# Optimization experiments

Hardware: AMD Instinct MI355X
Metric: run time of the kernel (lower is better)

## Reference

```python
import jax, jax.numpy as jnp
import numpy as np

B, C, H, W = 2, 512, 128, 128
L_NUM, HEADS, LEVELS, POINTS = 6, 8, 1, 4
HEAD_DIM = C // HEADS


def setup_inputs() -> dict:
    key = jax.random.key(0)
    ks = jax.random.split(key, 16)
    s = 0.02
    rn = lambda k, shape, scale=s: jax.random.normal(k, shape, jnp.float32) * scale
    return dict(
        bev_feat=jax.random.normal(ks[0], (B, C, H, W), jnp.float32),
        lidar_feat=jax.random.normal(ks[1], (B, C, H, W), jnp.float32),
        Wv=rn(ks[2], (L_NUM, C, C)), bv=jnp.zeros((L_NUM, C), jnp.float32),
        Woff=rn(ks[3], (L_NUM, C, HEADS * LEVELS * POINTS * 2)),
        boff=rn(ks[4], (L_NUM, HEADS * LEVELS * POINTS * 2), 0.5),
        Waw=rn(ks[5], (L_NUM, C, HEADS * LEVELS * POINTS)),
        baw=jnp.zeros((L_NUM, HEADS * LEVELS * POINTS), jnp.float32),
        Wout=rn(ks[6], (L_NUM, C, C)), bout=jnp.zeros((L_NUM, C), jnp.float32),
        ln1_g=jnp.ones((L_NUM, C), jnp.float32), ln1_b=jnp.zeros((L_NUM, C), jnp.float32),
        W1=rn(ks[7], (L_NUM, C, C)), W2=rn(ks[8], (L_NUM, C, C)),
        ln2_g=jnp.ones((L_NUM, C), jnp.float32), ln2_b=jnp.zeros((L_NUM, C), jnp.float32),
        pe_W1=rn(ks[9], (2, C), 0.5),
        pe_bn_g=jnp.ones((C,), jnp.float32), pe_bn_b=jnp.zeros((C,), jnp.float32),
        pe_bn_m=jnp.zeros((C,), jnp.float32), pe_bn_v=jnp.ones((C,), jnp.float32),
        pe_W2=rn(ks[10], (C, C)),
    )


def _layer_norm(x, g, b):
    mu = jnp.mean(x, -1, keepdims=True)
    var = jnp.mean((x - mu) ** 2, -1, keepdims=True)
    return (x - mu) * jax.lax.rsqrt(var + 1e-5) * g + b


def _bilinear_gather(v_flat, locx, locy):
    # v_flat: (B, heads, H*W, d); locx/locy: (B, heads, S) normalized [0,1]
    # grid_sample semantics: align_corners=False, zero padding
    x = locx * W - 0.5
    y = locy * H - 0.5
    x0f = jnp.floor(x); y0f = jnp.floor(y)
    wx = x - x0f; wy = y - y0f
    x0 = x0f.astype(jnp.int32); y0 = y0f.astype(jnp.int32)

    def corner(xi, yi, w):
        inb = (xi >= 0) & (xi < W) & (yi >= 0) & (yi < H)
        idx = jnp.clip(yi, 0, H - 1) * W + jnp.clip(xi, 0, W - 1)
        g = jnp.take_along_axis(v_flat, idx[..., None], axis=2)
        return g * (w * inb)[..., None]

    return (corner(x0, y0, (1 - wx) * (1 - wy)) + corner(x0 + 1, y0, wx * (1 - wy))
            + corner(x0, y0 + 1, (1 - wx) * wy) + corner(x0 + 1, y0 + 1, wx * wy))


def reference(bev_feat, lidar_feat, Wv, bv, Woff, boff, Waw, baw, Wout, bout,
              ln1_g, ln1_b, W1, W2, ln2_g, ln2_b,
              pe_W1, pe_bn_g, pe_bn_b, pe_bn_m, pe_bn_v, pe_W2):
    N = H * W
    # sparse voxelization: keep rows with all-nonzero features, pack valid-first per batch
    lf = jnp.transpose(lidar_feat, (0, 2, 3, 1)).reshape(B, N, C)
    mask = jnp.all(lf != 0, axis=-1)                       # (B,N)
    order = jnp.argsort((~mask).astype(jnp.int32), axis=1, stable=True)  # valid first
    valid = jnp.take_along_axis(mask, order, axis=1)       # (B,N)
    q = jnp.take_along_axis(lf, order[..., None], axis=1) * valid[..., None]
    hh = jnp.arange(N) // W
    ww = jnp.arange(N) % W
    ref_all = jnp.stack([ww / W, hh / H], -1).astype(jnp.float32)  # (N,2) = (x,y)
    ref = jnp.broadcast_to(ref_all, (B, N, 2))
    ref = jnp.take_along_axis(ref, order[..., None], axis=1) * valid[..., None]
    # learned positional embedding (BatchNorm in eval mode)
    pe = ref.reshape(B * N, 2) @ pe_W1
    pe = (pe - pe_bn_m) * jax.lax.rsqrt(pe_bn_v + 1e-5) * pe_bn_g + pe_bn_b
    q_pos = (jax.nn.relu(pe) @ pe_W2).reshape(B, N, C)
    feat_flat = jnp.transpose(bev_feat.reshape(B, C, N), (0, 2, 1))  # (B,N,C)
    norm_xy = jnp.array([W, H], jnp.float32)  # offset normalizer per level (w,h)
    for i in range(L_NUM):
        ident = q
        x = q + q_pos
        v = (feat_flat @ Wv[i] + bv[i]).reshape(B, N, HEADS, HEAD_DIM)
        v_flat = jnp.transpose(v, (0, 2, 1, 3))  # (B,heads,N,d)
        off = (x @ Woff[i] + boff[i]).reshape(B, N, HEADS, LEVELS * POINTS, 2)
        aw = jax.nn.softmax((x @ Waw[i] + baw[i]).reshape(B, N, HEADS, LEVELS * POINTS), axis=-1)
        loc = ref[:, :, None, None, :] + off / norm_xy      # (B,N,heads,P,2)
        locx = jnp.transpose(loc[..., 0], (0, 2, 1, 3)).reshape(B, HEADS, N * POINTS)
        locy = jnp.transpose(loc[..., 1], (0, 2, 1, 3)).reshape(B, HEADS, N * POINTS)
        samp = _bilinear_gather(v_flat, locx, locy).reshape(B, HEADS, N, POINTS, HEAD_DIM)
        awt = jnp.transpose(aw, (0, 2, 1, 3))               # (B,heads,N,P)
        out = jnp.sum(samp * awt[..., None], axis=3)        # (B,heads,N,d)
        out = jnp.transpose(out, (0, 2, 1, 3)).reshape(B, N, C)
        q = out @ Wout[i] + bout[i] + ident                 # dropout in eval = identity
        q = _layer_norm(q, ln1_g[i], ln1_b[i])
        q = jax.nn.relu(q @ W1[i]) @ W2[i] + q
        q = _layer_norm(q, ln2_g[i], ln2_b[i])
    # scatter back to dense (B,C,H,W); invalid voxels stay zero
    slots = jnp.zeros((B, N, C), q.dtype)
    slots = slots.at[jnp.arange(B)[:, None], order].set(q * valid[..., None])
    return jnp.transpose(slots.reshape(B, H, W, C), (0, 3, 1, 2))
```

## Files before the change

kernel.cpp:

```cpp
#include <hip/hip_runtime.h>
#include <cstdint>
#include <cstddef>

#define BDIM 2
#define CDIM 512
#define HDIM 128
#define WDIM 128
#define NDIM (HDIM * WDIM)
#define LNUM 6
#define NHEADS 8
#define HEAD_DIM 64
#define NPTS 4
#define BN_TOT (BDIM * NDIM)

typedef unsigned short u16;
typedef __attribute__((ext_vector_type(8))) short bf16x8;
typedef __attribute__((ext_vector_type(4))) float f32x4;

__device__ __forceinline__ u16 f2bf(float x) {
    unsigned u = __float_as_uint(x);
    u += 0x7fffu + ((u >> 16) & 1u);
    return (u16)(u >> 16);
}
__device__ __forceinline__ float bf2f(u16 h) {
    return __uint_as_float(((unsigned)h) << 16);
}

__device__ __forceinline__ void load_lds16(const void* g, void* l) {
    __builtin_amdgcn_global_load_lds(
        (const __attribute__((address_space(1))) void*)g,
        (__attribute__((address_space(3))) void*)l, 16, 0, 0);
}

__device__ __forceinline__ void wait_vm8() { asm volatile("s_waitcnt vmcnt(8)" ::: "memory"); }
__device__ __forceinline__ void wait_vm5() { asm volatile("s_waitcnt vmcnt(5)" ::: "memory"); }
__device__ __forceinline__ void wait_vm4() { asm volatile("s_waitcnt vmcnt(4)" ::: "memory"); }
__device__ __forceinline__ void wait_vm0() { asm volatile("s_waitcnt vmcnt(0)" ::: "memory"); }
__device__ __forceinline__ void sbar()  { __builtin_amdgcn_s_barrier(); }
__device__ __forceinline__ void spin()  { __builtin_amdgcn_sched_barrier(0); }

__global__ void mask_kernel(const float* __restrict__ lidar, int* __restrict__ mask)
{
    int idx = blockIdx.x * blockDim.x + threadIdx.x;
    if (idx >= BN_TOT) return;
    int b = idx / NDIM;
    int n = idx - b * NDIM;
    const float* p = lidar + (size_t)b * CDIM * NDIM + n;
    int ok = 1;
#pragma unroll 8
    for (int c = 0; c < CDIM; ++c)
        ok &= (p[(size_t)c * NDIM] != 0.0f);
    mask[idx] = ok;
}

__global__ void order_kernel(const int* __restrict__ mask, int* __restrict__ order,
                             int* __restrict__ nvalid)
{
    int b = blockIdx.x;
    const int* m = mask + b * NDIM;
    int* ord = order + b * NDIM;
    __shared__ int part[256];
    __shared__ int totalValid;
    int t = threadIdx.x;
    const int CHUNK = NDIM / 256;
    int base = t * CHUNK;
    int cnt = 0;
    for (int i = 0; i < CHUNK; ++i) cnt += m[base + i];
    part[t] = cnt;
    __syncthreads();
    for (int s = 1; s < 256; s <<= 1) {
        int v = (t >= s) ? part[t - s] : 0;
        __syncthreads();
        part[t] += v;
        __syncthreads();
    }
    if (t == 255) { totalValid = part[255]; nvalid[b] = part[255]; }
    __syncthreads();
    int validBefore = (t == 0) ? 0 : part[t - 1];
    int nv = totalValid;
    for (int i = 0; i < CHUNK; ++i) {
        int n = base + i;
        if (m[n]) { ord[validBefore] = n; validBefore++; }
        else      { int invBefore = n - validBefore; ord[nv + invBefore] = n; }
    }
}

__global__ void ref_kernel(const int* __restrict__ order, const int* __restrict__ nvalid,
                           float* __restrict__ ref)
{
    int idx = blockIdx.x * blockDim.x + threadIdx.x;
    if (idx >= BN_TOT) return;
    int b = idx / NDIM;
    int j = idx - b * NDIM;
    int n = order[idx];
    float flag = (j < nvalid[b]) ? 1.0f : 0.0f;
    int hh = n / WDIM;
    int ww = n - hh * WDIM;
    ref[(size_t)idx * 2 + 0] = ((float)ww / (float)WDIM) * flag;
    ref[(size_t)idx * 2 + 1] = ((float)hh / (float)HDIM) * flag;
}

__global__ void pack_q_kernel(const float* __restrict__ lidar, const int* __restrict__ order,
                              const int* __restrict__ nvalid, u16* __restrict__ q)
{
    __shared__ float tile[32][33];
    __shared__ int ord_s[32];
    int b  = blockIdx.z;
    int j0 = blockIdx.x * 32;
    int c0 = blockIdx.y * 32;
    int tx = threadIdx.x, ty = threadIdx.y;
    if (ty == 0) ord_s[tx] = order[b * NDIM + j0 + tx];
    __syncthreads();
    const float* src = lidar + (size_t)b * CDIM * NDIM;
#pragma unroll
    for (int k = 0; k < 4; ++k) {
        int cl = ty * 4 + k;
        tile[cl][tx] = src[(size_t)(c0 + cl) * NDIM + ord_s[tx]];
    }
    __syncthreads();
    int nv = nvalid[b];
#pragma unroll
    for (int k = 0; k < 4; ++k) {
        int jl = ty * 4 + k;
        int j = j0 + jl;
        float f = (j < nv) ? 1.0f : 0.0f;
        q[((size_t)b * NDIM + j) * CDIM + c0 + tx] = f2bf(tile[tx][jl] * f);
    }
}

__global__ void scatter_kernel(const u16* __restrict__ q, const int* __restrict__ order,
                               const int* __restrict__ nvalid, float* __restrict__ out)
{
    __shared__ float tile[32][33];
    __shared__ int ord_s[32];
    int b  = blockIdx.z;
    int j0 = blockIdx.x * 32;
    int c0 = blockIdx.y * 32;
    int tx = threadIdx.x, ty = threadIdx.y;
    if (ty == 0) ord_s[tx] = order[b * NDIM + j0 + tx];
    __syncthreads();
    int nv = nvalid[b];
#pragma unroll
    for (int k = 0; k < 4; ++k) {
        int jl = ty * 4 + k;
        int j = j0 + jl;
        float f = (j < nv) ? 1.0f : 0.0f;
        tile[jl][tx] = bf2f(q[((size_t)b * NDIM + j) * CDIM + c0 + tx]) * f;
    }
    __syncthreads();
    float* dst = out + (size_t)b * CDIM * NDIM;
#pragma unroll
    for (int k = 0; k < 4; ++k) {
        int cl = ty * 4 + k;
        dst[(size_t)(c0 + cl) * NDIM + ord_s[tx]] = tile[tx][cl];
    }
}

__global__ void tconv_b_kernel(const float* __restrict__ src0, u16* __restrict__ dst0)
{
    __shared__ float t[32][33];
    int z = blockIdx.z;
    const float* src = src0 + (size_t)z * 512 * 512;
    u16* dst = dst0 + (size_t)z * 512 * 512;
    int k0 = blockIdx.x * 32, n0 = blockIdx.y * 32;
    int tx = threadIdx.x, ty = threadIdx.y;
#pragma unroll
    for (int j = 0; j < 4; ++j) {
        int kl = ty * 4 + j;
        t[kl][tx] = src[(size_t)(k0 + kl) * 512 + n0 + tx];
    }
    __syncthreads();
#pragma unroll
    for (int j = 0; j < 4; ++j) {
        int nl = ty * 4 + j;
        dst[(size_t)(n0 + nl) * 512 + k0 + tx] = f2bf(t[tx][nl]);
    }
}

__global__ void tconv_offaw_b_kernel(const float* __restrict__ woff0,
                                     const float* __restrict__ waw0,
                                     u16* __restrict__ dst0)
{
    __shared__ float t[32][33];
    int z = blockIdx.z;
    const float* woff = woff0 + (size_t)z * 512 * 64;
    const float* waw  = waw0 + (size_t)z * 512 * 32;
    u16* dst = dst0 + (size_t)z * 96 * 512;
    int k0 = blockIdx.x * 32, n0 = blockIdx.y * 32;
    int tx = threadIdx.x, ty = threadIdx.y;
#pragma unroll
    for (int j = 0; j < 4; ++j) {
        int kl = ty * 4 + j;
        int n = n0 + tx;
        float v = (n < 64) ? woff[(size_t)(k0 + kl) * 64 + n]
                           : waw[(size_t)(k0 + kl) * 32 + (n - 64)];
        t[kl][tx] = v;
    }
    __syncthreads();
#pragma unroll
    for (int j = 0; j < 4; ++j) {
        int nl = ty * 4 + j;
        dst[(size_t)(n0 + nl) * 512 + k0 + tx] = f2bf(t[tx][nl]);
    }
}

__global__ void bev_conv_kernel(const float* __restrict__ bev, u16* __restrict__ dst)
{
    __shared__ float t[32][33];
    int b  = blockIdx.z;
    int n0 = blockIdx.x * 32;
    int c0 = blockIdx.y * 32;
    int tx = threadIdx.x, ty = threadIdx.y;
    const float* src = bev + (size_t)b * CDIM * NDIM;
#pragma unroll
    for (int j = 0; j < 4; ++j) {
        int cl = ty * 4 + j;
        t[cl][tx] = src[(size_t)(c0 + cl) * NDIM + n0 + tx];
    }
    __syncthreads();
#pragma unroll
    for (int j = 0; j < 4; ++j) {
        int nl = ty * 4 + j;
        dst[((size_t)b * NDIM + n0 + nl) * CDIM + c0 + tx] = f2bf(t[tx][nl]);
    }
}

__global__ void pe_hidden_kernel(const float* __restrict__ ref, const float* __restrict__ W1,
                                 const float* __restrict__ g, const float* __restrict__ bb,
                                 const float* __restrict__ m, const float* __restrict__ v,
                                 u16* __restrict__ out)
{
    int row = blockIdx.x;
    float r0 = ref[(size_t)row * 2 + 0];
    float r1 = ref[(size_t)row * 2 + 1];
    for (int c = threadIdx.x; c < CDIM; c += blockDim.x) {
        float pe = r0 * W1[c] + r1 * W1[CDIM + c];
        pe = (pe - m[c]) * rsqrtf(v[c] + 1e-5f) * g[c] + bb[c];
        out[(size_t)row * CDIM + c] = f2bf(fmaxf(pe, 0.0f));
    }
}

__global__ void add_bf_kernel(const u16* __restrict__ q, const u16* __restrict__ qpos,
                              u16* __restrict__ x)
{
    size_t i = (size_t)blockIdx.x * blockDim.x + threadIdx.x;
    uint4 qa = ((const uint4*)q)[i];
    uint4 pv = ((const uint4*)qpos)[i];
    unsigned qw[4] = {qa.x, qa.y, qa.z, qa.w};
    unsigned pw[4] = {pv.x, pv.y, pv.z, pv.w};
    unsigned rw[4];
#pragma unroll
    for (int k = 0; k < 4; ++k) {
        float a0 = bf2f((u16)(qw[k] & 0xffff)), a1 = bf2f((u16)(qw[k] >> 16));
        float p0 = bf2f((u16)(pw[k] & 0xffff)), p1 = bf2f((u16)(pw[k] >> 16));
        rw[k] = (unsigned)f2bf(a0 + p0) | ((unsigned)f2bf(a1 + p1) << 16);
    }
    uint4 r; r.x = rw[0]; r.y = rw[1]; r.z = rw[2]; r.w = rw[3];
    ((uint4*)x)[i] = r;
}

__global__ __launch_bounds__(256) void gemm_bf16(
    const u16* __restrict__ A, const u16* __restrict__ Bt,
    const float* __restrict__ bias, u16* __restrict__ outB, int relu)
{
    __shared__ u16 As[2][128 * 32];
    __shared__ u16 Bs[2][128 * 32];
    int tid = threadIdx.x;
    int wave = tid >> 6, lane = tid & 63;
    int wr = wave >> 1, wc = wave & 1;
    int quad = lane >> 4, l15 = lane & 15;
    int bm = blockIdx.y * 128, bn = blockIdx.x * 128;

    f32x4 acc[4][4];
#pragma unroll
    for (int i = 0; i < 4; ++i)
#pragma unroll
        for (int j = 0; j < 4; ++j) { f32x4 z = {0.f, 0.f, 0.f, 0.f}; acc[i][j] = z; }

    int ch0 = wave, ch1 = wave + 4;
    const u16* Ag0 = A  + (size_t)(bm + ch0 * 16 + (lane >> 2)) * 512 + (lane & 3) * 8;
    const u16* Ag1 = A  + (size_t)(bm + ch1 * 16 + (lane >> 2)) * 512 + (lane & 3) * 8;
    const u16* Bg0 = Bt + (size_t)(bn + ch0 * 16 + (lane >> 2)) * 512 + (lane & 3) * 8;
    const u16* Bg1 = Bt + (size_t)(bn + ch1 * 16 + (lane >> 2)) * 512 + (lane & 3) * 8;

    load_lds16(Ag0, &As[0][ch0 * 512]);
    load_lds16(Ag1, &As[0][ch1 * 512]);
    load_lds16(Bg0, &Bs[0][ch0 * 512]);
    load_lds16(Bg1, &Bs[0][ch1 * 512]);

    for (int it = 0; it < 16; ++it) {
        sbar();  spin();
        int cur = it & 1, nxt = cur ^ 1;
        if (it < 15) {
            int kn = (it + 1) * 32;
            load_lds16(Ag0 + kn, &As[nxt][ch0 * 512]);
            load_lds16(Ag1 + kn, &As[nxt][ch1 * 512]);
            load_lds16(Bg0 + kn, &Bs[nxt][ch0 * 512]);
            load_lds16(Bg1 + kn, &Bs[nxt][ch1 * 512]);
            wait_vm4();
        } else {
            wait_vm0();
        }
        sbar();  spin();
        bf16x8 av[4], bv[4];
#pragma unroll
        for (int mi = 0; mi < 4; ++mi)
            av[mi] = *(const bf16x8*)&As[cur][(wr * 64 + mi * 16 + l15) * 32 + quad * 8];
#pragma unroll
        for (int ni = 0; ni < 4; ++ni)
            bv[ni] = *(const bf16x8*)&Bs[cur][(wc * 64 + ni * 16 + l15) * 32 + quad * 8];
#pragma unroll
        for (int mi = 0; mi < 4; ++mi)
#pragma unroll
            for (int ni = 0; ni < 4; ++ni)
                acc[mi][ni] = __builtin_amdgcn_mfma_f32_16x16x32_bf16(
                    av[mi], bv[ni], acc[mi][ni], 0, 0, 0);
    }

    int rowb = bm + wr * 64;
    int colb = bn + wc * 64;
#pragma unroll
    for (int mi = 0; mi < 4; ++mi) {
#pragma unroll
        for (int ni = 0; ni < 4; ++ni) {
            int col = colb + ni * 16 + l15;
            float bi = bias ? bias[col] : 0.0f;
#pragma unroll
            for (int r = 0; r < 4; ++r) {
                int row = rowb + mi * 16 + quad * 4 + r;
                float val = acc[mi][ni][r] + bi;
                if (relu) val = fmaxf(val, 0.0f);
                outB[(size_t)row * 512 + col] = f2bf(val);
            }
        }
    }
}

__global__ __launch_bounds__(512) void gemm_ln(
    const u16* __restrict__ A, const u16* __restrict__ Bt,
    const float* __restrict__ bias, const u16* __restrict__ resid,
    const float* __restrict__ g, const float* __restrict__ bta,
    u16* __restrict__ outQ, const u16* __restrict__ qpos, u16* __restrict__ outX)
{
    __shared__ u16 As[2][128 * 32];
    __shared__ u16 Bs[2][512 * 32];
    __shared__ float rs[8][64];
    __shared__ float rq[8][64];
    __shared__ float muL[128], invL[128];

    int tid = threadIdx.x;
    int wv = tid >> 6, lane = tid & 63;
    int quad = lane >> 4, l15 = lane & 15;
    int wr = wv >> 2, wc = wv & 3;
    int bm = blockIdx.x * 128;

    f32x4 acc[4][8];
#pragma unroll
    for (int i = 0; i < 4; ++i)
#pragma unroll
        for (int j = 0; j < 8; ++j) { f32x4 z = {0.f, 0.f, 0.f, 0.f}; acc[i][j] = z; }

    const u16* Ag = A + (size_t)(bm + wv * 16 + (lane >> 2)) * 512 + (lane & 3) * 8;
    const u16* Bg[4];
#pragma unroll
    for (int s = 0; s < 4; ++s)
        Bg[s] = Bt + (size_t)((wv * 4 + s) * 16 + (lane >> 2)) * 512 + (lane & 3) * 8;

    load_lds16(Ag, &As[0][wv * 512]);
#pragma unroll
    for (int s = 0; s < 4; ++s)
        load_lds16(Bg[s], &Bs[0][(wv * 4 + s) * 512]);

    for (int kk = 0; kk < 16; ++kk) {
        sbar();  spin();
        int cur = kk & 1, nxt = cur ^ 1;
        if (kk < 15) {
            int kn = (kk + 1) * 32;
            load_lds16(Ag + kn, &As[nxt][wv * 512]);
#pragma unroll
            for (int s = 0; s < 4; ++s)
                load_lds16(Bg[s] + kn, &Bs[nxt][(wv * 4 + s) * 512]);
            wait_vm5();
        } else {
            wait_vm0();
        }
        sbar();  spin();
        bf16x8 av[4], bv[8];
#pragma unroll
        for (int mi = 0; mi < 4; ++mi)
            av[mi] = *(const bf16x8*)&As[cur][(wr * 64 + mi * 16 + l15) * 32 + quad * 8];
#pragma unroll
        for (int ni = 0; ni < 8; ++ni)
            bv[ni] = *(const bf16x8*)&Bs[cur][(wc * 128 + ni * 16 + l15) * 32 + quad * 8];
#pragma unroll
        for (int mi = 0; mi < 4; ++mi)
#pragma unroll
            for (int ni = 0; ni < 8; ++ni)
                acc[mi][ni] = __builtin_amdgcn_mfma_f32_16x16x32_bf16(
                    av[mi], bv[ni], acc[mi][ni], 0, 0, 0);
    }

    int colb = wc * 128;
    float biasv[8], gv[8], btv[8];
#pragma unroll
    for (int ni = 0; ni < 8; ++ni) {
        int c = colb + ni * 16 + l15;
        biasv[ni] = bias ? bias[c] : 0.0f;
        gv[ni] = g[c];
        btv[ni] = bta[c];
    }
#pragma unroll
    for (int mi = 0; mi < 4; ++mi) {
#pragma unroll
        for (int r = 0; r < 4; ++r) {
            size_t rowoff = (size_t)(bm + wr * 64 + mi * 16 + quad * 4 + r) * 512;
#pragma unroll
            for (int ni = 0; ni < 8; ++ni) {
                int col = colb + ni * 16 + l15;
                acc[mi][ni][r] += biasv[ni] + bf2f(resid[rowoff + col]);
            }
        }
    }
#pragma unroll
    for (int mi = 0; mi < 4; ++mi) {
#pragma unroll
        for (int r = 0; r < 4; ++r) {
            float s = 0.f, s2 = 0.f;
#pragma unroll
            for (int ni = 0; ni < 8; ++ni) {
                s  += acc[mi][ni][r];
                s2 += acc[mi][ni][r] * acc[mi][ni][r];
            }
#pragma unroll
            for (int m = 1; m < 16; m <<= 1) {
                s  += __shfl_xor(s, m, 64);
                s2 += __shfl_xor(s2, m, 64);
            }
            if (l15 == 0) {
                rs[wv][mi * 16 + quad * 4 + r] = s;
                rq[wv][mi * 16 + quad * 4 + r] = s2;
            }
        }
    }
    __syncthreads();
    if (tid < 128) {
        int wrg = tid >> 6, lr = tid & 63;
        float s = 0.f, s2 = 0.f;
#pragma unroll
        for (int w4 = 0; w4 < 4; ++w4) {
            int w = wrg * 4 + w4;
            s += rs[w][lr]; s2 += rq[w][lr];
        }
        float mu = s * (1.0f / 512.0f);
        float var = s2 * (1.0f / 512.0f) - mu * mu;
        muL[tid] = mu;
        invL[tid] = rsqrtf(var + 1e-5f);
    }
    __syncthreads();
#pragma unroll
    for (int mi = 0; mi < 4; ++mi) {
#pragma unroll
        for (int r = 0; r < 4; ++r) {
            int lrow = wr * 64 + mi * 16 + quad * 4 + r;
            float mu = muL[lrow], iv = invL[lrow];
            size_t rowoff = (size_t)(bm + lrow) * 512;
#pragma unroll
            for (int ni = 0; ni < 8; ++ni) {
                int col = colb + ni * 16 + l15;
                float y = (acc[mi][ni][r] - mu) * iv * gv[ni] + btv[ni];
                outQ[rowoff + col] = f2bf(y);
                if (outX)
                    outX[rowoff + col] = f2bf(y + bf2f(qpos[rowoff + col]));
            }
        }
    }
}

__global__ __launch_bounds__(256) void gemm_offaw(
    const u16* __restrict__ A, const u16* __restrict__ Bt,
    const float* __restrict__ boff, const float* __restrict__ baw,
    u16* __restrict__ offb, u16* __restrict__ awb)
{
    __shared__ u16 As[2][128 * 32];
    __shared__ u16 Bs[2][128 * 32];
    int tid = threadIdx.x;
    int wave = tid >> 6, lane = tid & 63;
    int wr = wave >> 1, wc = wave & 1;
    int quad = lane >> 4, l15 = lane & 15;
    int bm = blockIdx.y * 128;

    f32x4 acc[4][4];
#pragma unroll
    for (int i = 0; i < 4; ++i)
#pragma unroll
        for (int j = 0; j < 4; ++j) { f32x4 z = {0.f, 0.f, 0.f, 0.f}; acc[i][j] = z; }

    const u16* Ag[4];
    const u16* Bg[4];
#pragma unroll
    for (int s = 0; s < 4; ++s) {
        Ag[s] = A + (size_t)(bm + wr * 64 + s * 16 + (lane >> 2)) * 512 + (lane & 3) * 8;
        int br = wc * 64 + s * 16 + (lane >> 2);
        if (br > 95) br = 95;
        Bg[s] = Bt + (size_t)br * 512 + (lane & 3) * 8;
    }

#pragma unroll
    for (int s = 0; s < 4; ++s) {
        load_lds16(Ag[s], &As[0][(wr * 4 + s) * 512]);
        load_lds16(Bg[s], &Bs[0][(wc * 4 + s) * 512]);
    }

    for (int it = 0; it < 16; ++it) {
        sbar();
        int cur = it & 1, nxt = cur ^ 1;
        if (it < 15) {
            int kn = (it + 1) * 32;
#pragma unroll
            for (int s = 0; s < 4; ++s) {
                load_lds16(Ag[s] + kn, &As[nxt][(wr * 4 + s) * 512]);
                load_lds16(Bg[s] + kn, &Bs[nxt][(wc * 4 + s) * 512]);
            }
            wait_vm8();
        } else {
            wait_vm0();
        }
        bf16x8 av[4], bv[4];
#pragma unroll
        for (int mi = 0; mi < 4; ++mi)
            av[mi] = *(const bf16x8*)&As[cur][(wr * 64 + mi * 16 + l15) * 32 + quad * 8];
#pragma unroll
        for (int ni = 0; ni < 4; ++ni)
            bv[ni] = *(const bf16x8*)&Bs[cur][(wc * 64 + ni * 16 + l15) * 32 + quad * 8];
#pragma unroll
        for (int mi = 0; mi < 4; ++mi)
#pragma unroll
            for (int ni = 0; ni < 4; ++ni)
                acc[mi][ni] = __builtin_amdgcn_mfma_f32_16x16x32_bf16(
                    av[mi], bv[ni], acc[mi][ni], 0, 0, 0);
    }

    int rowb = bm + wr * 64;
#pragma unroll
    for (int mi = 0; mi < 4; ++mi) {
#pragma unroll
        for (int ni = 0; ni < 4; ++ni) {
            int col = wc * 64 + ni * 16 + l15;
            if (col < 96) {
                float bi = (col < 64) ? boff[col] : baw[col - 64];
#pragma unroll
                for (int r = 0; r < 4; ++r) {
                    int row = rowb + mi * 16 + quad * 4 + r;
                    float val = acc[mi][ni][r] + bi;
                    if (col < 64) offb[(size_t)row * 64 + col] = f2bf(val);
                    else          awb[(size_t)row * 32 + (col - 64)] = f2bf(val);
                }
            }
        }
    }
}

__global__ __launch_bounds__(256) void sample_kernel(
    const float* __restrict__ ref, const u16* __restrict__ off,
    const u16* __restrict__ aw, const u16* __restrict__ v,
    u16* __restrict__ out)
{
    int bj = blockIdx.x * 4 + (threadIdx.x >> 6);
    int lane = threadIdx.x & 63;
    int h  = lane >> 3;
    int d8 = (lane & 7) * 8;
    int b  = bj >> 14;

    float rx = ref[(size_t)bj * 2 + 0];
    float ry = ref[(size_t)bj * 2 + 1];
    uint4 offv = *(const uint4*)(off + (size_t)bj * 64 + h * 8);
    uint2 awv  = *(const uint2*)(aw + (size_t)bj * 32 + h * 4);

    float l0 = bf2f((u16)(awv.x & 0xffff)), l1 = bf2f((u16)(awv.x >> 16));
    float l2 = bf2f((u16)(awv.y & 0xffff)), l3 = bf2f((u16)(awv.y >> 16));
    float mx = fmaxf(fmaxf(l0, l1), fmaxf(l2, l3));
    float e[4];
    e[0] = expf(l0 - mx); e[1] = expf(l1 - mx);
    e[2] = expf(l2 - mx); e[3] = expf(l3 - mx);
    float inv_es = 1.0f / (e[0] + e[1] + e[2] + e[3]);

    const u16* vb = v + (size_t)b * NDIM * CDIM + h * HEAD_DIM + d8;
    float acc[8] = {0.f, 0.f, 0.f, 0.f, 0.f, 0.f, 0.f, 0.f};
    unsigned ow[4] = {offv.x, offv.y, offv.z, offv.w};

#pragma unroll
    for (int p = 0; p < NPTS; ++p) {
        float ox = bf2f((u16)(ow[p] & 0xffff));
        float oy = bf2f((u16)(ow[p] >> 16));
        float X = rx * (float)WDIM + ox - 0.5f;
        float Y = ry * (float)HDIM + oy - 0.5f;
        float x0f = floorf(X), y0f = floorf(Y);
        float wx = X - x0f, wy = Y - y0f;
        int x0 = (int)x0f, y0 = (int)y0f;
        float ep = e[p];
#pragma unroll
        for (int cy = 0; cy < 2; ++cy) {
            int yy = y0 + cy;
            float wyc = cy ? wy : (1.0f - wy);
            int yin = (yy >= 0) & (yy < HDIM);
            int yc = min(max(yy, 0), HDIM - 1);
#pragma unroll
            for (int cx = 0; cx < 2; ++cx) {
                int xx = x0 + cx;
                float wxc = cx ? wx : (1.0f - wx);
                int xin = (xx >= 0) & (xx < WDIM);
                int xc = min(max(xx, 0), WDIM - 1);
                float wgt = ep * wyc * wxc * (float)(yin & xin);
                uint4 vv = *(const uint4*)(vb + (size_t)(yc * WDIM + xc) * CDIM);
                acc[0] += wgt * bf2f((u16)(vv.x & 0xffff));
                acc[1] += wgt * bf2f((u16)(vv.x >> 16));
                acc[2] += wgt * bf2f((u16)(vv.y & 0xffff));
                acc[3] += wgt * bf2f((u16)(vv.y >> 16));
                acc[4] += wgt * bf2f((u16)(vv.z & 0xffff));
                acc[5] += wgt * bf2f((u16)(vv.z >> 16));
                acc[6] += wgt * bf2f((u16)(vv.w & 0xffff));
                acc[7] += wgt * bf2f((u16)(vv.w >> 16));
            }
        }
    }
    uint4 r;
    r.x = (unsigned)f2bf(acc[0] * inv_es) | ((unsigned)f2bf(acc[1] * inv_es) << 16);
    r.y = (unsigned)f2bf(acc[2] * inv_es) | ((unsigned)f2bf(acc[3] * inv_es) << 16);
    r.z = (unsigned)f2bf(acc[4] * inv_es) | ((unsigned)f2bf(acc[5] * inv_es) << 16);
    r.w = (unsigned)f2bf(acc[6] * inv_es) | ((unsigned)f2bf(acc[7] * inv_es) << 16);
    *(uint4*)(out + (size_t)bj * CDIM + h * HEAD_DIM + d8) = r;
}

extern "C" void kernel_launch(void* const* d_in, const int* in_sizes, int n_in,
                              void* d_out, int out_size, void* d_ws, size_t ws_size,
                              hipStream_t stream)
{
    const float* bev   = (const float*)d_in[0];
    const float* lidar = (const float*)d_in[1];
    const float* Wv    = (const float*)d_in[2];
    const float* bv    = (const float*)d_in[3];
    const float* Woff  = (const float*)d_in[4];
    const float* boff  = (const float*)d_in[5];
    const float* Waw   = (const float*)d_in[6];
    const float* baw   = (const float*)d_in[7];
    const float* Wout  = (const float*)d_in[8];
    const float* bout  = (const float*)d_in[9];
    const float* ln1g  = (const float*)d_in[10];
    const float* ln1b  = (const float*)d_in[11];
    const float* W1    = (const float*)d_in[12];
    const float* W2    = (const float*)d_in[13];
    const float* ln2g  = (const float*)d_in[14];
    const float* ln2b  = (const float*)d_in[15];
    const float* peW1  = (const float*)d_in[16];
    const float* peg   = (const float*)d_in[17];
    const float* peb   = (const float*)d_in[18];
    const float* pem   = (const float*)d_in[19];
    const float* pev   = (const float*)d_in[20];
    const float* peW2  = (const float*)d_in[21];

    const size_t NC = (size_t)BN_TOT * CDIM;
    const size_t WSZ = 512 * 512;

    char* base = (char*)d_ws;
    u16* q      = (u16*)base;
    u16* actA   = (u16*)(base + NC * 2);
    u16* actB   = (u16*)(base + NC * 4);
    u16* wt     = (u16*)(base + NC * 6);
    u16* wtv    = wt;
    u16* wtout  = wt + 6 * WSZ;
    u16* wt1    = wt + 12 * WSZ;
    u16* wt2    = wt + 18 * WSZ;
    u16* wtpe   = wt + 24 * WSZ;
    u16* offawt = wt + 25 * WSZ;
    u16* offb   = offawt + 6 * 96 * 512;
    u16* awb    = offb + (size_t)BN_TOT * 64;
    float* refb = (float*)(awb + (size_t)BN_TOT * 32);
    int* mask   = (int*)(refb + (size_t)BN_TOT * 2);
    int* order  = mask + BN_TOT;
    int* nvalid = order + BN_TOT;

    u16* qpos_bf = (u16*)d_out;
    u16* featT   = (u16*)d_out + NC;

    dim3 blk328(32, 8);
    dim3 gemm_grid(4, 256);
    dim3 offaw_grid(1, 256);
    int  ln_grid = BN_TOT / 128;

    mask_kernel<<<BN_TOT / 256, 256, 0, stream>>>(lidar, mask);
    order_kernel<<<BDIM, 256, 0, stream>>>(mask, order, nvalid);
    ref_kernel<<<BN_TOT / 256, 256, 0, stream>>>(order, nvalid, refb);
    pack_q_kernel<<<dim3(NDIM / 32, CDIM / 32, BDIM), blk328, 0, stream>>>(lidar, order, nvalid, q);
    bev_conv_kernel<<<dim3(NDIM / 32, CDIM / 32, BDIM), blk328, 0, stream>>>(bev, featT);

    tconv_b_kernel<<<dim3(16, 16, 6), blk328, 0, stream>>>(Wv,   wtv);
    tconv_b_kernel<<<dim3(16, 16, 6), blk328, 0, stream>>>(Wout, wtout);
    tconv_b_kernel<<<dim3(16, 16, 6), blk328, 0, stream>>>(W1,   wt1);
    tconv_b_kernel<<<dim3(16, 16, 6), blk328, 0, stream>>>(W2,   wt2);
    tconv_b_kernel<<<dim3(16, 16, 1), blk328, 0, stream>>>(peW2, wtpe);
    tconv_offaw_b_kernel<<<dim3(16, 3, 6), blk328, 0, stream>>>(Woff, Waw, offawt);

    pe_hidden_kernel<<<BN_TOT, 128, 0, stream>>>(refb, peW1, peg, peb, pem, pev, actA);
    gemm_bf16<<<gemm_grid, 256, 0, stream>>>(actA, wtpe, nullptr, qpos_bf, 0);

    add_bf_kernel<<<(unsigned)(NC / 8 / 256), 256, 0, stream>>>(q, qpos_bf, actB);

    for (int i = 0; i < LNUM; ++i) {
        gemm_offaw<<<offaw_grid, 256, 0, stream>>>(actB, offawt + (size_t)i * 96 * 512,
                                                   boff + i * 64, baw + i * 32, offb, awb);
        gemm_bf16<<<gemm_grid, 256, 0, stream>>>(featT, wtv + (size_t)i * WSZ,
                                                 bv + i * CDIM, actA, 0);
        sample_kernel<<<BN_TOT / 4, 256, 0, stream>>>(refb, offb, awb, actA, actB);
        gemm_ln<<<ln_grid, 512, 0, stream>>>(actB, wtout + (size_t)i * WSZ, bout + i * CDIM,
                                             q, ln1g + i * CDIM, ln1b + i * CDIM,
                                             q, nullptr, nullptr);
        gemm_bf16<<<gemm_grid, 256, 0, stream>>>(q, wt1 + (size_t)i * WSZ, nullptr, actA, 1);
        gemm_ln<<<ln_grid, 512, 0, stream>>>(actA, wt2 + (size_t)i * WSZ, nullptr,
                                             q, ln2g + i * CDIM, ln2b + i * CDIM,
                                             q, qpos_bf,
                                             (i < LNUM - 1) ? actB : nullptr);
    }

    scatter_kernel<<<dim3(NDIM / 32, CDIM / 32, BDIM), blk328, 0, stream>>>(
        q, order, nvalid, (float*)d_out);
}
```

Measured before the change: 1.875 ms.

## Split fused GEMM+LayerNorm into tiled GEMM with fp32 output plus row LayerNorm kernel

Replaces the full-row 128x512 GEMM+LayerNorm kernel, which used 512 threads and a large register tile, with a standard 128x128-tiled GEMM that adds bias and residual and writes fp32. A separate wave-per-row LayerNorm kernel then normalizes the rows and writes bf16 q. The work is split into two halves so the fp32 scratch fits in the existing bf16 activation buffers. The qpos add becomes a separate add kernel. This trades the old kernel's low occupancy and only 256 blocks for higher GEMM parallelism, at the cost of extra fp32 global round-trips and more launches.

```diff
diff --git a/kernel.cpp b/kernel.cpp
--- a/kernel.cpp
+++ b/kernel.cpp
@@ -33,7 +33,6 @@
 }
 
 __device__ __forceinline__ void wait_vm8() { asm volatile("s_waitcnt vmcnt(8)" ::: "memory"); }
-__device__ __forceinline__ void wait_vm5() { asm volatile("s_waitcnt vmcnt(5)" ::: "memory"); }
 __device__ __forceinline__ void wait_vm4() { asm volatile("s_waitcnt vmcnt(4)" ::: "memory"); }
 __device__ __forceinline__ void wait_vm0() { asm volatile("s_waitcnt vmcnt(0)" ::: "memory"); }
 __device__ __forceinline__ void sbar()  { __builtin_amdgcn_s_barrier(); }
@@ -336,144 +335,124 @@
     }
 }
 
-__global__ __launch_bounds__(512) void gemm_ln(
+__global__ __launch_bounds__(256) void gemm_residf(
     const u16* __restrict__ A, const u16* __restrict__ Bt,
     const float* __restrict__ bias, const u16* __restrict__ resid,
-    const float* __restrict__ g, const float* __restrict__ bta,
-    u16* __restrict__ outQ, const u16* __restrict__ qpos, u16* __restrict__ outX)
+    float* __restrict__ outY)
 {
     __shared__ u16 As[2][128 * 32];
-    __shared__ u16 Bs[2][512 * 32];
-    __shared__ float rs[8][64];
-    __shared__ float rq[8][64];
-    __shared__ float muL[128], invL[128];
-
+    __shared__ u16 Bs[2][128 * 32];
     int tid = threadIdx.x;
-    int wv = tid >> 6, lane = tid & 63;
+    int wave = tid >> 6, lane = tid & 63;
+    int wr = wave >> 1, wc = wave & 1;
     int quad = lane >> 4, l15 = lane & 15;
-    int wr = wv >> 2, wc = wv & 3;
-    int bm = blockIdx.x * 128;
-
-    f32x4 acc[4][8];
+    int bm = blockIdx.y * 128, bn = blockIdx.x * 128;
+
+    f32x4 acc[4][4];
 #pragma unroll
     for (int i = 0; i < 4; ++i)
 #pragma unroll
-        for (int j = 0; j < 8; ++j) { f32x4 z = {0.f, 0.f, 0.f, 0.f}; acc[i][j] = z; }
-
-    const u16* Ag = A + (size_t)(bm + wv * 16 + (lane >> 2)) * 512 + (lane & 3) * 8;
-    const u16* Bg[4];
-#pragma unroll
-    for (int s = 0; s < 4; ++s)
-        Bg[s] = Bt + (size_t)((wv * 4 + s) * 16 + (lane >> 2)) * 512 + (lane & 3) * 8;
-
-    load_lds16(Ag, &As[0][wv * 512]);
-#pragma unroll
-    for (int s = 0; s < 4; ++s)
-        load_lds16(Bg[s], &Bs[0][(wv * 4 + s) * 512]);
-
-    for (int kk = 0; kk < 16; ++kk) {
+        for (int j = 0; j < 4; ++j) { f32x4 z = {0.f, 0.f, 0.f, 0.f}; acc[i][j] = z; }
+
+    int ch0 = wave, ch1 = wave + 4;
+    const u16* Ag0 = A  + (size_t)(bm + ch0 * 16 + (lane >> 2)) * 512 + (lane & 3) * 8;
+    const u16* Ag1 = A  + (size_t)(bm + ch1 * 16 + (lane >> 2)) * 512 + (lane & 3) * 8;
+    const u16* Bg0 = Bt + (size_t)(bn + ch0 * 16 + (lane >> 2)) * 512 + (lane & 3) * 8;
+    const u16* Bg1 = Bt + (size_t)(bn + ch1 * 16 + (lane >> 2)) * 512 + (lane & 3) * 8;
+
+    load_lds16(Ag0, &As[0][ch0 * 512]);
+    load_lds16(Ag1, &As[0][ch1 * 512]);
+    load_lds16(Bg0, &Bs[0][ch0 * 512]);
+    load_lds16(Bg1, &Bs[0][ch1 * 512]);
+
+    for (int it = 0; it < 16; ++it) {
         sbar();  spin();
-        int cur = kk & 1, nxt = cur ^ 1;
-        if (kk < 15) {
-            int kn = (kk + 1) * 32;
-            load_lds16(Ag + kn, &As[nxt][wv * 512]);
-#pragma unroll
-            for (int s = 0; s < 4; ++s)
-                load_lds16(Bg[s] + kn, &Bs[nxt][(wv * 4 + s) * 512]);
-            wait_vm5();
+        int cur = it & 1, nxt = cur ^ 1;
+        if (it < 15) {
+            int kn = (it + 1) * 32;
+            load_lds16(Ag0 + kn, &As[nxt][ch0 * 512]);
+            load_lds16(Ag1 + kn, &As[nxt][ch1 * 512]);
+            load_lds16(Bg0 + kn, &Bs[nxt][ch0 * 512]);
+            load_lds16(Bg1 + kn, &Bs[nxt][ch1 * 512]);
+            wait_vm4();
         } else {
             wait_vm0();
         }
         sbar();  spin();
-        bf16x8 av[4], bv[8];
+        bf16x8 av[4], bv[4];
 #pragma unroll
         for (int mi = 0; mi < 4; ++mi)
             av[mi] = *(const bf16x8*)&As[cur][(wr * 64 + mi * 16 + l15) * 32 + quad * 8];
 #pragma unroll
-        for (int ni = 0; ni < 8; ++ni)
-            bv[ni] = *(const bf16x8*)&Bs[cur][(wc * 128 + ni * 16 + l15) * 32 + quad * 8];
+        for (int ni = 0; ni < 4; ++ni)
+            bv[ni] = *(const bf16x8*)&Bs[cur][(wc * 64 + ni * 16 + l15) * 32 + quad * 8];
 #pragma unroll
         for (int mi = 0; mi < 4; ++mi)
 #pragma unroll
-            for (int ni = 0; ni < 8; ++ni)
+            for (int ni = 0; ni < 4; ++ni)
                 acc[mi][ni] = __builtin_amdgcn_mfma_f32_16x16x32_bf16(
                     av[mi], bv[ni], acc[mi][ni], 0, 0, 0);
     }
 
-    int colb = wc * 128;
-    float biasv[8], gv[8], btv[8];
-#pragma unroll
-    for (int ni = 0; ni < 8; ++ni) {
-        int c = colb + ni * 16 + l15;
-        biasv[ni] = bias ? bias[c] : 0.0f;
-        gv[ni] = g[c];
-        btv[ni] = bta[c];
-    }
+    int rowb = bm + wr * 64;
+    int colb = bn + wc * 64;
 #pragma unroll
     for (int mi = 0; mi < 4; ++mi) {
 #pragma unroll
-        for (int r = 0; r < 4; ++r) {
-            size_t rowoff = (size_t)(bm + wr * 64 + mi * 16 + quad * 4 + r) * 512;
-#pragma unroll
-            for (int ni = 0; ni < 8; ++ni) {
-                int col = colb + ni * 16 + l15;
-                acc[mi][ni][r] += biasv[ni] + bf2f(resid[rowoff + col]);
+        for (int ni = 0; ni < 4; ++ni) {
+            int col = colb + ni * 16 + l15;
+            float bi = bias ? bias[col] : 0.0f;
+#pragma unroll
+            for (int r = 0; r < 4; ++r) {
+                int row = rowb + mi * 16 + quad * 4 + r;
+                size_t off = (size_t)row * 512 + col;
+                outY[off] = acc[mi][ni][r] + bi + bf2f(resid[off]);
             }
         }
     }
-#pragma unroll
-    for (int mi = 0; mi < 4; ++mi) {
-#pragma unroll
-        for (int r = 0; r < 4; ++r) {
-            float s = 0.f, s2 = 0.f;
-#pragma unroll
-            for (int ni = 0; ni < 8; ++ni) {
-                s  += acc[mi][ni][r];
-                s2 += acc[mi][ni][r] * acc[mi][ni][r];
-            }
-#pragma unroll
-            for (int m = 1; m < 16; m <<= 1) {
-                s  += __shfl_xor(s, m, 64);
-                s2 += __shfl_xor(s2, m, 64);
-            }
-            if (l15 == 0) {
-                rs[wv][mi * 16 + quad * 4 + r] = s;
-                rq[wv][mi * 16 + quad * 4 + r] = s2;
-            }
-        }
-    }
-    __syncthreads();
-    if (tid < 128) {
-        int wrg = tid >> 6, lr = tid & 63;
-        float s = 0.f, s2 = 0.f;
-#pragma unroll
-        for (int w4 = 0; w4 < 4; ++w4) {
-            int w = wrg * 4 + w4;
-            s += rs[w][lr]; s2 += rq[w][lr];
-        }
-        float mu = s * (1.0f / 512.0f);
-        float var = s2 * (1.0f / 512.0f) - mu * mu;
-        muL[tid] = mu;
-        invL[tid] = rsqrtf(var + 1e-5f);
-    }
-    __syncthreads();
-#pragma unroll
-    for (int mi = 0; mi < 4; ++mi) {
-#pragma unroll
-        for (int r = 0; r < 4; ++r) {
-            int lrow = wr * 64 + mi * 16 + quad * 4 + r;
-            float mu = muL[lrow], iv = invL[lrow];
-            size_t rowoff = (size_t)(bm + lrow) * 512;
-#pragma unroll
-            for (int ni = 0; ni < 8; ++ni) {
-                int col = colb + ni * 16 + l15;
-                float y = (acc[mi][ni][r] - mu) * iv * gv[ni] + btv[ni];
-                outQ[rowoff + col] = f2bf(y);
-                if (outX)
-                    outX[rowoff + col] = f2bf(y + bf2f(qpos[rowoff + col]));
-            }
-        }
-    }
+}
+
+__global__ __launch_bounds__(256) void ln_f(
+    const float* __restrict__ Y, const float* __restrict__ g,
+    const float* __restrict__ bta, u16* __restrict__ outQ)
+{
+    int row  = blockIdx.x * 4 + (threadIdx.x >> 6);
+    int lane = threadIdx.x & 63;
+    size_t base = (size_t)row * CDIM + lane * 8;
+
+    float4 y0 = *(const float4*)(Y + base);
+    float4 y1 = *(const float4*)(Y + base + 4);
+    float v[8] = {y0.x, y0.y, y0.z, y0.w, y1.x, y1.y, y1.z, y1.w};
+
+    float s = 0.f, s2 = 0.f;
+#pragma unroll
+    for (int j = 0; j < 8; ++j) { s += v[j]; s2 += v[j] * v[j]; }
+#pragma unroll
+    for (int m = 1; m < 64; m <<= 1) {
+        s  += __shfl_xor(s, m, 64);
+        s2 += __shfl_xor(s2, m, 64);
+    }
+    float mu = s * (1.0f / 512.0f);
+    float var = s2 * (1.0f / 512.0f) - mu * mu;
+    float iv = rsqrtf(var + 1e-5f);
+
+    int c0 = lane * 8;
+    float4 g0 = *(const float4*)(g + c0);
+    float4 g1 = *(const float4*)(g + c0 + 4);
+    float4 b0 = *(const float4*)(bta + c0);
+    float4 b1 = *(const float4*)(bta + c0 + 4);
+    float gl[8] = {g0.x, g0.y, g0.z, g0.w, g1.x, g1.y, g1.z, g1.w};
+    float bl[8] = {b0.x, b0.y, b0.z, b0.w, b1.x, b1.y, b1.z, b1.w};
+
+    unsigned qw[4];
+#pragma unroll
+    for (int k = 0; k < 4; ++k) {
+        float a = (v[2 * k]     - mu) * iv * gl[2 * k]     + bl[2 * k];
+        float b = (v[2 * k + 1] - mu) * iv * gl[2 * k + 1] + bl[2 * k + 1];
+        qw[k] = (unsigned)f2bf(a) | ((unsigned)f2bf(b) << 16);
+    }
+    uint4 qo; qo.x = qw[0]; qo.y = qw[1]; qo.z = qw[2]; qo.w = qw[3];
+    *(uint4*)(outQ + base) = qo;
 }
 
 __global__ __launch_bounds__(256) void gemm_offaw(
@@ -656,15 +635,18 @@
     const float* peb   = (const float*)d_in[18];
     const float* pem   = (const float*)d_in[19];
     const float* pev   = (const float*)d_in[20];
-    const float* peW2  = (const float*)d_in[21];
-
-    const size_t NC = (size_t)BN_TOT * CDIM;
-    const size_t WSZ = 512 * 512;
+    const float* pe_W2 = (const float*)d_in[21];
+
+    const size_t NC   = (size_t)BN_TOT * CDIM;
+    const size_t HALF = NC / 2;
+    const size_t WSZ  = 512 * 512;
 
     char* base = (char*)d_ws;
     u16* q      = (u16*)base;
     u16* actA   = (u16*)(base + NC * 2);
     u16* actB   = (u16*)(base + NC * 4);
+    float* actAf = (float*)actA;
+    float* actBf = (float*)actB;
     u16* wt     = (u16*)(base + NC * 6);
     u16* wtv    = wt;
     u16* wtout  = wt + 6 * WSZ;
@@ -684,8 +666,10 @@
 
     dim3 blk328(32, 8);
     dim3 gemm_grid(4, 256);
+    dim3 gemm_half(4, 128);
     dim3 offaw_grid(1, 256);
-    int  ln_grid = BN_TOT / 128;
+    int  lnf_half = (BN_TOT / 2) / 4;
+    unsigned addb = (unsigned)(NC / 8 / 256);
 
     mask_kernel<<<BN_TOT / 256, 256, 0, stream>>>(lidar, mask);
     order_kernel<<<BDIM, 256, 0, stream>>>(mask, order, nvalid);
@@ -697,13 +681,13 @@
     tconv_b_kernel<<<dim3(16, 16, 6), blk328, 0, stream>>>(Wout, wtout);
     tconv_b_kernel<<<dim3(16, 16, 6), blk328, 0, stream>>>(W1,   wt1);
     tconv_b_kernel<<<dim3(16, 16, 6), blk328, 0, stream>>>(W2,   wt2);
-    tconv_b_kernel<<<dim3(16, 16, 1), blk328, 0, stream>>>(peW2, wtpe);
+    tconv_b_kernel<<<dim3(16, 16, 1), blk328, 0, stream>>>(pe_W2, wtpe);
     tconv_offaw_b_kernel<<<dim3(16, 3, 6), blk328, 0, stream>>>(Woff, Waw, offawt);
 
     pe_hidden_kernel<<<BN_TOT, 128, 0, stream>>>(refb, peW1, peg, peb, pem, pev, actA);
     gemm_bf16<<<gemm_grid, 256, 0, stream>>>(actA, wtpe, nullptr, qpos_bf, 0);
 
-    add_bf_kernel<<<(unsigned)(NC / 8 / 256), 256, 0, stream>>>(q, qpos_bf, actB);
+    add_bf_kernel<<<addb, 256, 0, stream>>>(q, qpos_bf, actB);
 
     for (int i = 0; i < LNUM; ++i) {
         gemm_offaw<<<offaw_grid, 256, 0, stream>>>(actB, offawt + (size_t)i * 96 * 512,
@@ -711,14 +695,23 @@
         gemm_bf16<<<gemm_grid, 256, 0, stream>>>(featT, wtv + (size_t)i * WSZ,
                                                  bv + i * CDIM, actA, 0);
         sample_kernel<<<BN_TOT / 4, 256, 0, stream>>>(refb, offb, awb, actA, actB);
-        gemm_ln<<<ln_grid, 512, 0, stream>>>(actB, wtout + (size_t)i * WSZ, bout + i * CDIM,
-                                             q, ln1g + i * CDIM, ln1b + i * CDIM,
-                                             q, nullptr, nullptr);
+        for (int c = 0; c < 2; ++c) {
+            gemm_residf<<<gemm_half, 256, 0, stream>>>(
+                actB + c * HALF, wtout + (size_t)i * WSZ, bout + i * CDIM,
+                q + c * HALF, actAf);
+            ln_f<<<lnf_half, 256, 0, stream>>>(
+                actAf, ln1g + i * CDIM, ln1b + i * CDIM, q + c * HALF);
+        }
         gemm_bf16<<<gemm_grid, 256, 0, stream>>>(q, wt1 + (size_t)i * WSZ, nullptr, actA, 1);
-        gemm_ln<<<ln_grid, 512, 0, stream>>>(actA, wt2 + (size_t)i * WSZ, nullptr,
-                                             q, ln2g + i * CDIM, ln2b + i * CDIM,
-                                             q, qpos_bf,
-                                             (i < LNUM - 1) ? actB : nullptr);
+        for (int c = 0; c < 2; ++c) {
+            gemm_residf<<<gemm_half, 256, 0, stream>>>(
+                actA + c * HALF, wt2 + (size_t)i * WSZ, nullptr,
+                q + c * HALF, actBf);
+            ln_f<<<lnf_half, 256, 0, stream>>>(
+                actBf, ln2g + i * CDIM, ln2b + i * CDIM, q + c * HALF);
+        }
+        if (i < LNUM - 1)
+            add_bf_kernel<<<addb, 256, 0, stream>>>(q, qpos_bf, actB);
     }
 
     scatter_kernel<<<dim3(NDIM / 32, CDIM / 32, BDIM), blk328, 0, stream>>>(
```

Measured after the change: 1.850 ms. No clear change (-1.3%).
